# Performance work log

Hardware: AMD Instinct MI355X
Metric: run time of the kernel (lower is better)

Reference implementation:

```python
import jax, jax.numpy as jnp
import numpy as np

NUM_USERS = 400000  # matches fill_max of indexes in input_specs
K = 10              # top_k from init_kwargs
NEG_INF = -1000000000.0


def setup_inputs() -> dict:
    key = jax.random.key(0)
    k1, k2, k3 = jax.random.split(key, 3)
    N = 8000000
    predictions = jax.random.normal(k1, (N,), dtype=jnp.float32)
    targets = jax.random.uniform(k2, (N,), dtype=jnp.float32)
    indexes = jax.random.randint(k3, (N,), 0, NUM_USERS, dtype=jnp.int64)
    return {"predictions": predictions, "targets": targets, "indexes": indexes}


def reference(predictions, targets, indexes):
    # Faithful to the torch source, which does `counts_per_user[u] = 1` (not +=1):
    # column 0 holds each user's FIRST occurrence, column 1 holds the LAST
    # occurrence (subsequent scatters to pos 1 overwrite), everything else is
    # padding (-1e9 preds / 0 targets). Padding columns beyond k provably don't
    # affect topk/dcg/idcg, so we use a static width of K.
    n = predictions.shape[0]
    pos = jnp.arange(n, dtype=jnp.int32)
    seg = indexes.astype(jnp.int32)
    first = jax.ops.segment_min(pos, seg, num_segments=NUM_USERS)
    last = jax.ops.segment_max(pos, seg, num_segments=NUM_USERS)
    counts = jax.ops.segment_sum(jnp.ones_like(pos), seg, num_segments=NUM_USERS)
    has2 = counts >= 2  # pos 1 is only ever written on a second occurrence

    p0 = predictions[first]
    t0 = targets[first]
    p1 = jnp.where(has2, predictions[last], NEG_INF)
    t1 = jnp.where(has2, targets[last], 0.0)

    pred_padded = jnp.full((NUM_USERS, K), NEG_INF, dtype=predictions.dtype)
    pred_padded = pred_padded.at[:, 0].set(p0).at[:, 1].set(p1)
    target_padded = jnp.zeros((NUM_USERS, K), dtype=targets.dtype)
    target_padded = target_padded.at[:, 0].set(t0).at[:, 1].set(t1)

    _, topk_idx = jax.lax.top_k(pred_padded, K)
    topk_targets = jnp.take_along_axis(target_padded, topk_idx, axis=1)
    discounts = jnp.log2(jnp.arange(2, K + 2, dtype=jnp.float32))
    dcg = (topk_targets / discounts).sum(axis=1)
    ideal = -jnp.sort(-target_padded, axis=1)  # descending sort
    idcg = (ideal[:, :K] / discounts).sum(axis=1)
    return (dcg / idcg).mean()
```

## Files before the change

### kernel.cpp

```cpp
#include <hip/hip_runtime.h>
#include <climits>

static constexpr int NUSERS = 400000;
static constexpr float NEG_INF_F = -1000000000.0f;
static constexpr float INV_LOG2_3 = 0.6309297535714575f;

static constexpr int USLICE_LOG = 12;
static constexpr int USLICE = 1 << USLICE_LOG;
static constexpr int S = 98;
static constexpr int CHUNK = 4096;
static constexpr int CPG = 255;
static constexpr int GSPAN = CHUNK * CPG;
static constexpr int G = 8;
static constexpr int CAP = 12288;
static constexpr int B_B = 6;


__global__ void k_init_part(int* __restrict__ cursor, float* __restrict__ acc) {
    int t = blockIdx.x * blockDim.x + threadIdx.x;
    if (t < G * S) cursor[t] = 0;
    if (t == G * S) acc[0] = 0.0f;
}

__global__ __launch_bounds__(256, 6) void k_scatter(const int* __restrict__ idx, int n,
                                                    unsigned* __restrict__ records,
                                                    int* __restrict__ cursor) {
    __shared__ int cnt[S];
    __shared__ int base_l[S + 1];
    __shared__ int base_g[S];
    __shared__ unsigned stage[CHUNK];
    __shared__ unsigned char stage_s[CHUNK];

    const int t = threadIdx.x;
    const int g = blockIdx.x / CPG;
    const int gbase = g * GSPAN;
    const int q0 = blockIdx.x * (CHUNK / 4);
    const int nq = n >> 2;
    const int4* idx4 = reinterpret_cast<const int4*>(idx);

    int4 v[4];
    int rnk[16];
#pragma unroll
    for (int k = 0; k < 4; ++k) {
        int q = q0 + k * 256 + t;
        v[k] = (q < nq) ? idx4[q] : make_int4(-1, -1, -1, -1);
    }

    if (t < S) cnt[t] = 0;
    __syncthreads();

#pragma unroll
    for (int k = 0; k < 4; ++k) {
        int us[4] = {v[k].x, v[k].y, v[k].z, v[k].w};
#pragma unroll
        for (int e = 0; e < 4; ++e)
            rnk[k * 4 + e] = (us[e] >= 0) ? atomicAdd(&cnt[us[e] >> USLICE_LOG], 1) : 0;
    }
    __syncthreads();

    if (t < 64) {
        int a0 = cnt[t];
        int b0 = (64 + t < S) ? cnt[64 + t] : 0;
        int a = a0, b = b0;
#pragma unroll
        for (int d = 1; d < 64; d <<= 1) {
            int y = __shfl_up(a, d, 64);
            if (t >= d) a += y;
        }
        int tot_a = __shfl(a, 63, 64);
#pragma unroll
        for (int d = 1; d < 64; d <<= 1) {
            int y = __shfl_up(b, d, 64);
            if (t >= d) b += y;
        }
        b += tot_a;
        base_l[t] = a - a0;
        if (64 + t < S) base_l[64 + t] = b - b0;
        if (t == (S - 1 - 64)) base_l[S] = b;
    }
    if (t < S) base_g[t] = atomicAdd(&cursor[g * S + t], cnt[t]);
    __syncthreads();

#pragma unroll
    for (int k = 0; k < 4; ++k) {
        int q = q0 + k * 256 + t;
        int us[4] = {v[k].x, v[k].y, v[k].z, v[k].w};
#pragma unroll
        for (int e = 0; e < 4; ++e) {
            int u = us[e];
            if (u >= 0) {
                int s = u >> USLICE_LOG;
                int pos = base_l[s] + rnk[k * 4 + e];
                unsigned iloc = (unsigned)(q * 4 + e - gbase);
                stage[pos] = ((unsigned)(u & (USLICE - 1)) << 20) | iloc;
                stage_s[pos] = (unsigned char)s;
            }
        }
    }
    __syncthreads();

    int total = base_l[S];
    for (int r = t; r < total; r += 256) {
        unsigned rec = stage[r];
        int s = stage_s[r];
        int pos = base_g[s] + (r - base_l[s]);
        if (pos < CAP)
            records[(size_t)(g * S + s) * CAP + pos] = rec;
    }
}

__global__ __launch_bounds__(256, 4) void k_reduce(const unsigned* __restrict__ records,
                                                   const int* __restrict__ cursor,
                                                   int2* __restrict__ partials) {
    __shared__ int tabf[USLICE];
    __shared__ int tabl[USLICE];
    const int s = blockIdx.x / B_B;
    const int j = blockIdx.x % B_B;
    const int t = threadIdx.x;

    for (int u = t; u < USLICE; u += 256) { tabf[u] = INT_MAX; tabl[u] = -1; }

    int cnts[G];
#pragma unroll
    for (int g = 0; g < G; ++g) cnts[g] = min(cursor[g * S + s], CAP);

    auto load_grp = [&](int g, uint4* dst) {
        int cnt = cnts[g];
        int per = (((cnt + B_B - 1) / B_B) + 3) & ~3;
        int lo = j * per;
        int hi = min(cnt, lo + per);
        const uint4* base4 = reinterpret_cast<const uint4*>(records + (size_t)(g * S + s) * CAP);
#pragma unroll
        for (int w = 0; w < 2; ++w) {
            int p = lo + (w * 256 + t) * 4;
            dst[w] = (p < hi) ? base4[p >> 2] : make_uint4(0, 0, 0, 0);
        }
    };

    uint4 cur[2], nxt[2];
    load_grp(0, cur);
    __syncthreads();

    for (int g = 0; g < G; ++g) {
        if (g + 1 < G) load_grp(g + 1, nxt);
        int cnt = cnts[g];
        int per = (((cnt + B_B - 1) / B_B) + 3) & ~3;
        int lo = j * per;
        int hi = min(cnt, lo + per);
        const int gb = g * GSPAN;
#pragma unroll
        for (int w = 0; w < 2; ++w) {
            int p = lo + (w * 256 + t) * 4;
            unsigned rec[4] = {cur[w].x, cur[w].y, cur[w].z, cur[w].w};
#pragma unroll
            for (int e = 0; e < 4; ++e) {
                if (p + e < hi) {
                    int loc = rec[e] >> 20;
                    int i = (int)(rec[e] & 0xFFFFFu) + gb;
                    atomicMin(&tabf[loc], i);
                    atomicMax(&tabl[loc], i);
                }
            }
        }
        cur[0] = nxt[0]; cur[1] = nxt[1];
    }
    __syncthreads();

    int2* out = partials + (size_t)blockIdx.x * USLICE;
    for (int u = t; u < USLICE; u += 256) out[u] = make_int2(tabf[u], tabl[u]);
}

__global__ void k_ndcg_part(const float* __restrict__ pred, const float* __restrict__ tgt,
                            const int2* __restrict__ partials, int n,
                            float* __restrict__ acc) {
    int u = blockIdx.x * blockDim.x + threadIdx.x;
    float v = 0.0f;
    if (u < NUSERS) {
        int s = u >> USLICE_LOG;
        int loc = u & (USLICE - 1);
        int f = INT_MAX, l = -1;
        const int2* p = partials + (size_t)(s * B_B) * USLICE + loc;
#pragma unroll
        for (int j = 0; j < B_B; ++j) {
            int2 e = p[(size_t)j * USLICE];
            f = min(f, e.x);
            l = max(l, e.y);
        }
        f = min(f, n - 1);
        float p0 = pred[f];
        float t0 = tgt[f];
        bool has2 = l > f;
        float p1 = has2 ? pred[l] : NEG_INF_F;
        float t1 = has2 ? tgt[l] : 0.0f;
        float dcg  = (p0 >= p1) ? fmaf(t1, INV_LOG2_3, t0) : fmaf(t0, INV_LOG2_3, t1);
        float idcg = fmaf(fminf(t0, t1), INV_LOG2_3, fmaxf(t0, t1));
        v = dcg / idcg;
    }
    for (int off = 32; off > 0; off >>= 1) v += __shfl_down(v, off, 64);
    __shared__ float wsum[4];
    int lane = threadIdx.x & 63;
    int wid = threadIdx.x >> 6;
    if (lane == 0) wsum[wid] = v;
    __syncthreads();
    if (threadIdx.x == 0) atomicAdd(acc, wsum[0] + wsum[1] + wsum[2] + wsum[3]);
}

__global__ void k_final(const float* __restrict__ acc, float* __restrict__ out) {
    out[0] = acc[0] * (1.0f / (float)NUSERS);
}


__global__ void k_init_fb(int* __restrict__ first, int* __restrict__ last,
                          float* __restrict__ acc) {
    int i = blockIdx.x * blockDim.x + threadIdx.x;
    if (i < NUSERS) { first[i] = INT_MAX; last[i] = -1; }
    if (i == 0) acc[0] = 0.0f;
}

__global__ void k_minmax_fb(const int* __restrict__ idx, int* __restrict__ first,
                            int* __restrict__ last, int n) {
    int base = (blockIdx.x * blockDim.x + threadIdx.x) * 4;
    if (base + 3 < n) {
        int4 u4 = *reinterpret_cast<const int4*>(idx + base);
        int us[4] = {u4.x, u4.y, u4.z, u4.w};
#pragma unroll
        for (int j = 0; j < 4; ++j) {
            int u = us[j], i = base + j;
            if (i < first[u]) atomicMin(&first[u], i);
            if (i > last[u])  atomicMax(&last[u], i);
        }
    } else {
        for (int i = base; i < n; ++i) {
            int u = idx[i];
            if (i < first[u]) atomicMin(&first[u], i);
            if (i > last[u])  atomicMax(&last[u], i);
        }
    }
}

__global__ void k_ndcg_fb(const float* __restrict__ pred, const float* __restrict__ tgt,
                          const int* __restrict__ first, const int* __restrict__ last,
                          int n, float* __restrict__ acc) {
    int u = blockIdx.x * blockDim.x + threadIdx.x;
    float v = 0.0f;
    if (u < NUSERS) {
        int f = min(first[u], n - 1);
        int l = last[u];
        float p0 = pred[f], t0 = tgt[f];
        bool has2 = l > f;
        float p1 = has2 ? pred[l] : NEG_INF_F;
        float t1 = has2 ? tgt[l] : 0.0f;
        float dcg  = (p0 >= p1) ? fmaf(t1, INV_LOG2_3, t0) : fmaf(t0, INV_LOG2_3, t1);
        float idcg = fmaf(fminf(t0, t1), INV_LOG2_3, fmaxf(t0, t1));
        v = dcg / idcg;
    }
    for (int off = 32; off > 0; off >>= 1) v += __shfl_down(v, off, 64);
    __shared__ float wsum[4];
    int lane = threadIdx.x & 63, wid = threadIdx.x >> 6;
    if (lane == 0) wsum[wid] = v;
    __syncthreads();
    if (threadIdx.x == 0) atomicAdd(acc, wsum[0] + wsum[1] + wsum[2] + wsum[3]);
}


extern "C" void kernel_launch(void* const* d_in, const int* in_sizes, int n_in,
                              void* d_out, int out_size, void* d_ws, size_t ws_size,
                              hipStream_t stream) {
    const float* pred = (const float*)d_in[0];
    const float* tgt  = (const float*)d_in[1];
    const int*   idx  = (const int*)d_in[2];
    const int n = in_sizes[0];
    float* out = (float*)d_out;

    const size_t recs_bytes = (size_t)G * S * CAP * sizeof(unsigned);
    const size_t part_bytes = (size_t)S * B_B * USLICE * sizeof(int2);
    const size_t need = recs_bytes + part_bytes + 8192 + 64;

    if (ws_size >= need && n <= G * GSPAN && (n & 3) == 0) {
        unsigned* records = (unsigned*)d_ws;
        int2* partials = (int2*)((char*)d_ws + recs_bytes);
        int* cursor = (int*)((char*)d_ws + recs_bytes + part_bytes);
        float* acc = (float*)((char*)d_ws + recs_bytes + part_bytes + 8192);

        k_init_part<<<(G * S + 256) / 256, 256, 0, stream>>>(cursor, acc);

        int nblocks = (n + CHUNK - 1) / CHUNK;
        k_scatter<<<nblocks, 256, 0, stream>>>(idx, n, records, cursor);

        k_reduce<<<S * B_B, 256, 0, stream>>>(records, cursor, partials);

        k_ndcg_part<<<(NUSERS + 255) / 256, 256, 0, stream>>>(pred, tgt, partials, n, acc);

        k_final<<<1, 1, 0, stream>>>(acc, out);
    } else {
        int* first = (int*)d_ws;
        int* last  = first + NUSERS;
        float* acc = (float*)(last + NUSERS);

        k_init_fb<<<(NUSERS + 255) / 256, 256, 0, stream>>>(first, last, acc);
        int nq4 = (n + 3) / 4;
        k_minmax_fb<<<(nq4 + 255) / 256, 256, 0, stream>>>(idx, first, last, n);
        k_ndcg_fb<<<(NUSERS + 255) / 256, 256, 0, stream>>>(pred, tgt, first, last, n, acc);
        k_final<<<1, 1, 0, stream>>>(acc, out);
    }
}
```

Baseline: 167.9 us.

## Fuse slice reduction with NDCG, halve slice width, drop partials buffer

Halves the user-slice width so there are twice as many slices, each covered by one 1024-thread block. That block reduces all groups' records for its slice into shared first/last tables and then computes the per-user NDCG directly, which removes the partials buffer and the separate NDCG kernel. This saves a launch and the global write and read of the partials. In exchange there are only 196 blocks with no split within a slice, so GPU occupancy and load balance may suffer. The scatter kernel's prefix scan is extended to cover four wavefront-sized segments to handle the larger slice count.

```diff
diff --git a/kernel.cpp b/kernel.cpp
--- a/kernel.cpp
+++ b/kernel.cpp
@@ -5,15 +5,14 @@
 static constexpr float NEG_INF_F = -1000000000.0f;
 static constexpr float INV_LOG2_3 = 0.6309297535714575f;
 
-static constexpr int USLICE_LOG = 12;
+static constexpr int USLICE_LOG = 11;
 static constexpr int USLICE = 1 << USLICE_LOG;
-static constexpr int S = 98;
+static constexpr int S = 196;
 static constexpr int CHUNK = 4096;
 static constexpr int CPG = 255;
 static constexpr int GSPAN = CHUNK * CPG;
 static constexpr int G = 8;
-static constexpr int CAP = 12288;
-static constexpr int B_B = 6;
+static constexpr int CAP = 6144;
 
 
 __global__ void k_init_part(int* __restrict__ cursor, float* __restrict__ acc) {
@@ -59,24 +58,29 @@
     __syncthreads();
 
     if (t < 64) {
-        int a0 = cnt[t];
-        int b0 = (64 + t < S) ? cnt[64 + t] : 0;
-        int a = a0, b = b0;
-#pragma unroll
-        for (int d = 1; d < 64; d <<= 1) {
-            int y = __shfl_up(a, d, 64);
-            if (t >= d) a += y;
-        }
-        int tot_a = __shfl(a, 63, 64);
-#pragma unroll
-        for (int d = 1; d < 64; d <<= 1) {
-            int y = __shfl_up(b, d, 64);
-            if (t >= d) b += y;
-        }
-        b += tot_a;
-        base_l[t] = a - a0;
-        if (64 + t < S) base_l[64 + t] = b - b0;
-        if (t == (S - 1 - 64)) base_l[S] = b;
+        int v0 = cnt[t];
+        int v1 = (64 + t < S) ? cnt[64 + t] : 0;
+        int v2 = (128 + t < S) ? cnt[128 + t] : 0;
+        int v3 = (192 + t < S) ? cnt[192 + t] : 0;
+        int a = v0, b = v1, c = v2, d = v3;
+#pragma unroll
+        for (int dd = 1; dd < 64; dd <<= 1) { int y = __shfl_up(a, dd, 64); if (t >= dd) a += y; }
+        int ta = __shfl(a, 63, 64);
+#pragma unroll
+        for (int dd = 1; dd < 64; dd <<= 1) { int y = __shfl_up(b, dd, 64); if (t >= dd) b += y; }
+        int tb = __shfl(b, 63, 64);
+#pragma unroll
+        for (int dd = 1; dd < 64; dd <<= 1) { int y = __shfl_up(c, dd, 64); if (t >= dd) c += y; }
+        int tc = __shfl(c, 63, 64);
+#pragma unroll
+        for (int dd = 1; dd < 64; dd <<= 1) { int y = __shfl_up(d, dd, 64); if (t >= dd) d += y; }
+        int td = __shfl(d, 63, 64);
+        b += ta; c += ta + tb; d += ta + tb + tc;
+        base_l[t] = a - v0;
+        if (64 + t < S)  base_l[64 + t]  = b - v1;
+        if (128 + t < S) base_l[128 + t] = c - v2;
+        if (192 + t < S) base_l[192 + t] = d - v3;
+        if (t == 0) base_l[S] = ta + tb + tc + td;
     }
     if (t < S) base_g[t] = atomicAdd(&cursor[g * S + t], cnt[t]);
     __syncthreads();
@@ -109,100 +113,67 @@
     }
 }
 
-__global__ __launch_bounds__(256, 4) void k_reduce(const unsigned* __restrict__ records,
-                                                   const int* __restrict__ cursor,
-                                                   int2* __restrict__ partials) {
+__global__ __launch_bounds__(1024, 4) void k_reduce_ndcg(
+        const unsigned* __restrict__ records, const int* __restrict__ cursor,
+        const float* __restrict__ pred, const float* __restrict__ tgt,
+        int n, float* __restrict__ acc) {
     __shared__ int tabf[USLICE];
     __shared__ int tabl[USLICE];
-    const int s = blockIdx.x / B_B;
-    const int j = blockIdx.x % B_B;
+    const int s = blockIdx.x;
     const int t = threadIdx.x;
 
-    for (int u = t; u < USLICE; u += 256) { tabf[u] = INT_MAX; tabl[u] = -1; }
-
-    int cnts[G];
-#pragma unroll
-    for (int g = 0; g < G; ++g) cnts[g] = min(cursor[g * S + s], CAP);
-
-    auto load_grp = [&](int g, uint4* dst) {
-        int cnt = cnts[g];
-        int per = (((cnt + B_B - 1) / B_B) + 3) & ~3;
-        int lo = j * per;
-        int hi = min(cnt, lo + per);
+    for (int u = t; u < USLICE; u += 1024) { tabf[u] = INT_MAX; tabl[u] = -1; }
+    __syncthreads();
+
+    for (int g = 0; g < G; ++g) {
+        int cnt = min(cursor[g * S + s], CAP);
         const uint4* base4 = reinterpret_cast<const uint4*>(records + (size_t)(g * S + s) * CAP);
-#pragma unroll
-        for (int w = 0; w < 2; ++w) {
-            int p = lo + (w * 256 + t) * 4;
-            dst[w] = (p < hi) ? base4[p >> 2] : make_uint4(0, 0, 0, 0);
-        }
-    };
-
-    uint4 cur[2], nxt[2];
-    load_grp(0, cur);
-    __syncthreads();
-
-    for (int g = 0; g < G; ++g) {
-        if (g + 1 < G) load_grp(g + 1, nxt);
-        int cnt = cnts[g];
-        int per = (((cnt + B_B - 1) / B_B) + 3) & ~3;
-        int lo = j * per;
-        int hi = min(cnt, lo + per);
         const int gb = g * GSPAN;
-#pragma unroll
-        for (int w = 0; w < 2; ++w) {
-            int p = lo + (w * 256 + t) * 4;
-            unsigned rec[4] = {cur[w].x, cur[w].y, cur[w].z, cur[w].w};
+        for (int p4 = t; p4 * 4 < cnt; p4 += 1024) {
+            uint4 vv = base4[p4];
+            int p = p4 * 4;
+            unsigned rr[4] = {vv.x, vv.y, vv.z, vv.w};
 #pragma unroll
             for (int e = 0; e < 4; ++e) {
-                if (p + e < hi) {
-                    int loc = rec[e] >> 20;
-                    int i = (int)(rec[e] & 0xFFFFFu) + gb;
+                if (p + e < cnt) {
+                    int loc = rr[e] >> 20;
+                    int i = (int)(rr[e] & 0xFFFFFu) + gb;
                     atomicMin(&tabf[loc], i);
                     atomicMax(&tabl[loc], i);
                 }
             }
         }
-        cur[0] = nxt[0]; cur[1] = nxt[1];
-    }
-    __syncthreads();
-
-    int2* out = partials + (size_t)blockIdx.x * USLICE;
-    for (int u = t; u < USLICE; u += 256) out[u] = make_int2(tabf[u], tabl[u]);
-}
-
-__global__ void k_ndcg_part(const float* __restrict__ pred, const float* __restrict__ tgt,
-                            const int2* __restrict__ partials, int n,
-                            float* __restrict__ acc) {
-    int u = blockIdx.x * blockDim.x + threadIdx.x;
+    }
+    __syncthreads();
+
     float v = 0.0f;
-    if (u < NUSERS) {
-        int s = u >> USLICE_LOG;
-        int loc = u & (USLICE - 1);
-        int f = INT_MAX, l = -1;
-        const int2* p = partials + (size_t)(s * B_B) * USLICE + loc;
-#pragma unroll
-        for (int j = 0; j < B_B; ++j) {
-            int2 e = p[(size_t)j * USLICE];
-            f = min(f, e.x);
-            l = max(l, e.y);
-        }
-        f = min(f, n - 1);
-        float p0 = pred[f];
-        float t0 = tgt[f];
-        bool has2 = l > f;
-        float p1 = has2 ? pred[l] : NEG_INF_F;
-        float t1 = has2 ? tgt[l] : 0.0f;
-        float dcg  = (p0 >= p1) ? fmaf(t1, INV_LOG2_3, t0) : fmaf(t0, INV_LOG2_3, t1);
-        float idcg = fmaf(fminf(t0, t1), INV_LOG2_3, fmaxf(t0, t1));
-        v = dcg / idcg;
+    for (int uu = t; uu < USLICE; uu += 1024) {
+        int u = s * USLICE + uu;
+        if (u < NUSERS) {
+            int f = tabf[uu];
+            int l = tabl[uu];
+            f = min(f, n - 1);
+            float p0 = pred[f];
+            float t0 = tgt[f];
+            bool has2 = l > f;
+            float p1 = has2 ? pred[l] : NEG_INF_F;
+            float t1 = has2 ? tgt[l] : 0.0f;
+            float dcg  = (p0 >= p1) ? fmaf(t1, INV_LOG2_3, t0) : fmaf(t0, INV_LOG2_3, t1);
+            float idcg = fmaf(fminf(t0, t1), INV_LOG2_3, fmaxf(t0, t1));
+            v += dcg / idcg;
+        }
     }
     for (int off = 32; off > 0; off >>= 1) v += __shfl_down(v, off, 64);
-    __shared__ float wsum[4];
-    int lane = threadIdx.x & 63;
-    int wid = threadIdx.x >> 6;
+    __shared__ float wsum[16];
+    int lane = t & 63, wid = t >> 6;
     if (lane == 0) wsum[wid] = v;
     __syncthreads();
-    if (threadIdx.x == 0) atomicAdd(acc, wsum[0] + wsum[1] + wsum[2] + wsum[3]);
+    if (t == 0) {
+        float ss = 0.0f;
+#pragma unroll
+        for (int w = 0; w < 16; ++w) ss += wsum[w];
+        atomicAdd(acc, ss);
+    }
 }
 
 __global__ void k_final(const float* __restrict__ acc, float* __restrict__ out) {
@@ -273,23 +244,19 @@
     float* out = (float*)d_out;
 
     const size_t recs_bytes = (size_t)G * S * CAP * sizeof(unsigned);
-    const size_t part_bytes = (size_t)S * B_B * USLICE * sizeof(int2);
-    const size_t need = recs_bytes + part_bytes + 8192 + 64;
+    const size_t need = recs_bytes + 16384 + 64;
 
     if (ws_size >= need && n <= G * GSPAN && (n & 3) == 0) {
         unsigned* records = (unsigned*)d_ws;
-        int2* partials = (int2*)((char*)d_ws + recs_bytes);
-        int* cursor = (int*)((char*)d_ws + recs_bytes + part_bytes);
-        float* acc = (float*)((char*)d_ws + recs_bytes + part_bytes + 8192);
+        int* cursor = (int*)((char*)d_ws + recs_bytes);
+        float* acc = (float*)((char*)d_ws + recs_bytes + 16384);
 
         k_init_part<<<(G * S + 256) / 256, 256, 0, stream>>>(cursor, acc);
 
         int nblocks = (n + CHUNK - 1) / CHUNK;
         k_scatter<<<nblocks, 256, 0, stream>>>(idx, n, records, cursor);
 
-        k_reduce<<<S * B_B, 256, 0, stream>>>(records, cursor, partials);
-
-        k_ndcg_part<<<(NUSERS + 255) / 256, 256, 0, stream>>>(pred, tgt, partials, n, acc);
+        k_reduce_ndcg<<<S, 1024, 0, stream>>>(records, cursor, pred, tgt, n, acc);
 
         k_final<<<1, 1, 0, stream>>>(acc, out);
     } else {
```

After: 157.1 us. 6.4% less time.
